# Optimization experiments

Measured on AMD Instinct MI355X. Metric: run time of the kernel, lower is better.

## Reference

```python
import jax, jax.numpy as jnp
import numpy as np

B, S, V, H, NL, NH, FF, L = 32, 256, 30522, 768, 12, 12, 3072, 9
DH = H // NH
SCALE = 1.0 / float(np.sqrt(DH))

def _ln(x, g, b, eps=1e-12):
    mu = x.mean(-1, keepdims=True)
    var = ((x - mu) ** 2).mean(-1, keepdims=True)
    return (x - mu) * jax.lax.rsqrt(var + eps) * g + b

def _crf_nll(em, tags, mask, start, end, trans):
    # em: [B,S,L] log-softmaxed emissions; tags: [B,S] int; mask: [B,S] bool
    b, s, l = em.shape
    bi = jnp.arange(b)
    em_t = jnp.swapaxes(em, 0, 1)          # [S,B,L]
    tg_t = tags.T                           # [S,B]
    m_t = mask.T.astype(em.dtype)           # [S,B]
    # numerator: score of the gold path
    score0 = start[tags[:, 0]] + em[bi, 0, tags[:, 0]]
    def num_step(sc, xs):
        e, tg, tgp, m = xs
        return sc + m * (trans[tgp, tg] + e[bi, tg]), None
    num, _ = jax.lax.scan(num_step, score0, (em_t[1:], tg_t[1:], tg_t[:-1], m_t[1:]))
    seq_ends = mask.sum(1).astype(jnp.int32) - 1
    num = num + end[tags[bi, seq_ends]]
    # denominator: log partition via forward algorithm
    alpha0 = start[None, :] + em[:, 0]      # [B,L]
    def den_step(al, xs):
        e, m = xs
        new = jax.nn.logsumexp(al[:, :, None] + trans[None] + e[:, None, :], axis=1)
        return jnp.where(m[:, None] > 0, new, al), None
    alpha, _ = jax.lax.scan(den_step, alpha0, (em_t[1:], m_t[1:]))
    den = jax.nn.logsumexp(alpha + end[None, :], axis=1)
    return -(num - den).sum()   # torchcrf reduction='sum', negated in module

def _bert_crf_loss(token_ids, token_type_ids, attention_mask, y, p):
    b, s = token_ids.shape
    h = p['word_emb'][token_ids] + p['pos_emb'][:s][None] + p['type_emb'][token_type_ids]
    h = _ln(h, p['emb_ln_g'], p['emb_ln_b'])
    bias = (1.0 - attention_mask.astype(jnp.float32))[:, None, None, :] * -1e9
    def layer(hc, lp):
        Wq, bq, Wk, bk, Wv, bv, Wo, bo, g1, bln1, W1, b1, W2, b2, g2, bln2 = lp
        q = (hc @ Wq + bq).reshape(b, s, NH, DH)
        k = (hc @ Wk + bk).reshape(b, s, NH, DH)
        v = (hc @ Wv + bv).reshape(b, s, NH, DH)
        att = jnp.einsum('bqhd,bkhd->bhqk', q, k) * SCALE + bias
        att = jax.nn.softmax(att, axis=-1)
        ctx = jnp.einsum('bhqk,bkhd->bqhd', att, v).reshape(b, s, H)
        hc = _ln(hc + ctx @ Wo + bo, g1, bln1)
        ff = jax.nn.gelu(hc @ W1 + b1) @ W2 + b2
        hc = _ln(hc + ff, g2, bln2)
        return hc, None
    stacked = (p['Wq'], p['bq'], p['Wk'], p['bk'], p['Wv'], p['bv'], p['Wo'], p['bo'],
               p['ln1_g'], p['ln1_b'], p['W1'], p['b1'], p['W2'], p['b2'], p['ln2_g'], p['ln2_b'])
    h, _ = jax.lax.scan(layer, h, stacked)
    # dropout is identity in eval; fc has no bias; LogSoftmax over labels
    logits = jax.nn.log_softmax(h @ p['fc_w'], axis=-1)   # [B,S,L]
    return _crf_nll(logits, y, attention_mask.astype(bool), p['crf_start'], p['crf_end'], p['crf_trans'])

def setup_inputs() -> dict:
    key = jax.random.key(0)
    ks = iter(jax.random.split(key, 32))
    def nrm(shape, scale=0.02):
        return (jax.random.normal(next(ks), shape, jnp.float32) * scale)
    inp = dict(
        token_ids=jax.random.randint(next(ks), (B, S), 0, V),
        token_type_ids=jnp.zeros((B, S), jnp.int32),
        attention_mask=jnp.ones((B, S), jnp.int32),
        y=jax.random.randint(next(ks), (B, S), 0, L),
        word_emb=nrm((V, H)), pos_emb=nrm((S, H)), type_emb=nrm((2, H)),
        emb_ln_g=jnp.ones(H, jnp.float32), emb_ln_b=jnp.zeros(H, jnp.float32),
        Wq=nrm((NL, H, H)), bq=jnp.zeros((NL, H), jnp.float32),
        Wk=nrm((NL, H, H)), bk=jnp.zeros((NL, H), jnp.float32),
        Wv=nrm((NL, H, H)), bv=jnp.zeros((NL, H), jnp.float32),
        Wo=nrm((NL, H, H)), bo=jnp.zeros((NL, H), jnp.float32),
        ln1_g=jnp.ones((NL, H), jnp.float32), ln1_b=jnp.zeros((NL, H), jnp.float32),
        W1=nrm((NL, H, FF)), b1=jnp.zeros((NL, FF), jnp.float32),
        W2=nrm((NL, FF, H)), b2=jnp.zeros((NL, H), jnp.float32),
        ln2_g=jnp.ones((NL, H), jnp.float32), ln2_b=jnp.zeros((NL, H), jnp.float32),
        fc_w=nrm((H, L)),
        crf_start=nrm((L,), 0.1), crf_end=nrm((L,), 0.1), crf_trans=nrm((L, L), 0.1),
    )
    return inp

def reference(token_ids, token_type_ids, attention_mask, y, word_emb, pos_emb, type_emb,
              emb_ln_g, emb_ln_b, Wq, bq, Wk, bk, Wv, bv, Wo, bo, ln1_g, ln1_b,
              W1, b1, W2, b2, ln2_g, ln2_b, fc_w, crf_start, crf_end, crf_trans):
    p = dict(word_emb=word_emb, pos_emb=pos_emb, type_emb=type_emb,
             emb_ln_g=emb_ln_g, emb_ln_b=emb_ln_b, Wq=Wq, bq=bq, Wk=Wk, bk=bk,
             Wv=Wv, bv=bv, Wo=Wo, bo=bo, ln1_g=ln1_g, ln1_b=ln1_b,
             W1=W1, b1=b1, W2=W2, b2=b2, ln2_g=ln2_g, ln2_b=ln2_b,
             fc_w=fc_w, crf_start=crf_start, crf_end=crf_end, crf_trans=crf_trans)
    return _bert_crf_loss(token_ids, token_type_ids, attention_mask, y, p)
```

## Files before the change

### kernel.cpp

```cpp
#include <hip/hip_runtime.h>
#include <math.h>

typedef unsigned short ushortT;
typedef unsigned char u8;
typedef __attribute__((ext_vector_type(4))) float f32x4;
typedef __attribute__((ext_vector_type(4))) unsigned int u32x4;
typedef __attribute__((ext_vector_type(4))) unsigned short u16x4;
typedef __attribute__((ext_vector_type(4))) int i32x4;
typedef __attribute__((ext_vector_type(8))) __bf16 bf16x8;

namespace {
constexpr int S = 256;
constexpr int H = 768;
constexpr int NLAY = 12;
constexpr int NHD = 12;
constexpr int FF = 3072;
constexpr int LBL = 9;
constexpr int DH = 64;
constexpr int BATCH = 32;
constexpr int TOKENS = BATCH * S;
constexpr int QKVN = 3 * H;
constexpr float C2 = 0.18033688011112042f;

constexpr size_t HB_OFF  = 0;
constexpr size_t QB_OFF  = HB_OFF + (size_t)TOKENS*H/2;
constexpr size_t KB_OFF  = QB_OFF + (size_t)TOKENS*H/2;
constexpr size_t VT_OFF  = KB_OFF + (size_t)TOKENS*H/2;
constexpr size_t BIG_OFF = VT_OFF + (size_t)TOKENS*H/2;
constexpr size_t WTQ_OFF = BIG_OFF + (size_t)TOKENS*FF/2;
constexpr size_t WTO_OFF = WTQ_OFF + 3*(size_t)H*H/4;
constexpr size_t WT1_OFF = WTO_OFF + (size_t)H*H/4;
constexpr size_t WT2_OFF = WT1_OFF + (size_t)H*FF/4;
constexpr size_t EM_OFF  = WT2_OFF + (size_t)H*FF/4;
constexpr size_t PART_OFF= EM_OFF + (size_t)TOKENS*LBL;
constexpr size_t BQKV_OFF= PART_OFF + 64;
constexpr size_t H8_OFF  = BQKV_OFF + (size_t)NLAY*QKVN;
constexpr size_t CT8_OFF = H8_OFF + (size_t)TOKENS*H/4;
constexpr size_t WS_FLOATS = CT8_OFF + (size_t)TOKENS*H/4;
}

__device__ __forceinline__ ushortT f2bf(float x) {
    unsigned u = __builtin_bit_cast(unsigned, x);
    u += 0x7fffu + ((u >> 16) & 1u);
    return (ushortT)(u >> 16);
}
__device__ __forceinline__ float bf2f(ushortT h) {
    unsigned u = ((unsigned)h) << 16;
    return __builtin_bit_cast(float, u);
}
__device__ __forceinline__ u8 f2fp8(float x) {
    return (u8)(__builtin_amdgcn_cvt_pk_fp8_f32(x, x, 0, false) & 0xff);
}
__device__ __forceinline__ unsigned f2fp8x4(float a, float b, float c, float d) {
    int p = __builtin_amdgcn_cvt_pk_fp8_f32(a, b, 0, false);
    p = __builtin_amdgcn_cvt_pk_fp8_f32(c, d, p, true);
    return (unsigned)p;
}

__device__ __forceinline__ float exp2i(float x) {
    float r; asm("v_exp_f32 %0, %1" : "=v"(r) : "v"(x)); return r;
}
__device__ __forceinline__ float log2i(float x) {
    float r; asm("v_log_f32 %0, %1" : "=v"(r) : "v"(x)); return r;
}

__device__ __forceinline__ float gelu_tanh(float x) {
    float u = 0.7978845608028654f * (x + 0.044715f * x * x * x);
    float t = exp2i(-2.8853900817779268f * u);
    return x / (1.0f + t);
}

__device__ __forceinline__ f32x4 mfma16(u32x4 a, u32x4 b, f32x4 c) {
    return __builtin_amdgcn_mfma_f32_16x16x32_bf16(
        __builtin_bit_cast(bf16x8, a), __builtin_bit_cast(bf16x8, b), c, 0, 0, 0);
}

__device__ __forceinline__ void gload_lds16(const ushortT* g, ushortT* l) {
    __builtin_amdgcn_global_load_lds(
        (const __attribute__((address_space(1))) unsigned int*)g,
        (__attribute__((address_space(3))) unsigned int*)l,
        16, 0, 0);
}
__device__ __forceinline__ void gload_lds16b(const u8* g, u8* l) {
    __builtin_amdgcn_global_load_lds(
        (const __attribute__((address_space(1))) unsigned int*)g,
        (__attribute__((address_space(3))) unsigned int*)l,
        16, 0, 0);
}

template<int MODE>
__global__ __launch_bounds__(256) void gemm_fp8(
    const u8* __restrict__ A, int lda,
    const u8* __restrict__ Bt, int ldb,
    const float* __restrict__ bias,
    void* __restrict__ Cv, int ldc, int K)
{
    __shared__ __align__(16) u8 As[3][128 * 64];
    __shared__ __align__(16) u8 Bs[3][128 * 64];
    const int tid = threadIdx.x;
    const int wave = tid >> 6, lane = tid & 63;

    int bxi = blockIdx.x, byi = blockIdx.y;
    {
        const int nwg = gridDim.x * gridDim.y;
        const int lin = byi * gridDim.x + bxi;
        const int cpx = nwg >> 3;
        const int sw = (lin & 7) * cpx + (lin >> 3);
        byi = sw / gridDim.x; bxi = sw - byi * gridDim.x;
    }
    const int bm = byi * 128, bn = bxi * 128;
    const u8* Ab = A + (size_t)bm * lda;
    const u8* Bb = Bt + (size_t)bn * ldb;
    const int wm = wave >> 1, wn = wave & 1;

    const int lrow = lane >> 2;
    const int lswb = ((lane & 3) ^ ((lrow >> 1) & 3)) * 16;
    const int rl = lane & 15;
    const int kg = lane >> 4;
    const int kg4 = kg << 2;
    const int key = (rl >> 1) & 3;
    const int kgh = kg >> 1, kgl8 = (kg & 1) * 8;

    f32x4 acc[4][4];
#pragma unroll
    for (int i = 0; i < 4; ++i)
#pragma unroll
        for (int j = 0; j < 4; ++j) acc[i][j] = (f32x4){0.f, 0.f, 0.f, 0.f};

    auto stage = [&](int buf, int kt) {
#pragma unroll
        for (int j = 0; j < 2; ++j) {
            int chunk = j * 4 + wave;
            gload_lds16b(Ab + (size_t)(chunk * 16 + lrow) * lda + kt * 64 + lswb,
                         &As[buf][chunk * 1024]);
        }
#pragma unroll
        for (int j = 0; j < 2; ++j) {
            int chunk = j * 4 + wave;
            gload_lds16b(Bb + (size_t)(chunk * 16 + lrow) * ldb + kt * 64 + lswb,
                         &Bs[buf][chunk * 1024]);
        }
    };

    const int nt = K >> 6;
    stage(0, 0);
    stage(1, (nt > 1) ? 1 : 0);
    int cur = 0;
    for (int t = 0; t < nt; ++t) {
        asm volatile("s_waitcnt vmcnt(4)" ::: "memory");
        __builtin_amdgcn_s_barrier();
        __builtin_amdgcn_sched_barrier(0);
#pragma unroll
        for (int ks = 0; ks < 2; ++ks) {
            long a[4], b[4];
#pragma unroll
            for (int mf = 0; mf < 4; ++mf)
                a[mf] = *(const long*)&As[cur][(wm * 64 + mf * 16 + rl) * 64 +
                                               (((ks * 2 + kgh) ^ key) << 4) + kgl8];
#pragma unroll
            for (int nf = 0; nf < 4; ++nf)
                b[nf] = *(const long*)&Bs[cur][(wn * 64 + nf * 16 + rl) * 64 +
                                               (((ks * 2 + kgh) ^ key) << 4) + kgl8];
            if (ks == 0) {
                const int nx = (t + 2 < nt) ? t + 2 : nt - 1;
                int nb = cur + 2; if (nb >= 3) nb -= 3;
                stage(nb, nx);
            }
#pragma unroll
            for (int mf = 0; mf < 4; ++mf)
#pragma unroll
                for (int nf = 0; nf < 4; ++nf)
                    acc[mf][nf] = __builtin_amdgcn_mfma_f32_16x16x32_fp8_fp8(
                        a[mf], b[nf], acc[mf][nf], 0, 0, 0);
        }
        cur = (cur + 1 == 3) ? 0 : cur + 1;
    }
    asm volatile("s_waitcnt vmcnt(0)" ::: "memory");

#pragma unroll
    for (int nf = 0; nf < 4; ++nf) {
        const int gn = bn + wn * 64 + nf * 16 + rl;
        const float bv = bias[gn];
#pragma unroll
        for (int mf = 0; mf < 4; ++mf) {
            const int gm = bm + wm * 64 + mf * 16 + kg4;
            if constexpr (MODE == 7) {
                u8* C8 = (u8*)Cv;
#pragma unroll
                for (int r = 0; r < 4; ++r)
                    C8[(size_t)(gm + r) * ldc + gn] = f2fp8(gelu_tanh(acc[mf][nf][r] + bv));
            } else if constexpr (MODE == 9) {
                const int region = gn / H;
                const int col = gn - region * H;
                if (region < 2) {
                    ushortT* o = (ushortT*)Cv + (size_t)region * TOKENS * H;
#pragma unroll
                    for (int r = 0; r < 4; ++r)
                        o[(size_t)(gm + r) * H + col] = f2bf(acc[mf][nf][r] + bv);
                } else {
                    u16x4 o;
#pragma unroll
                    for (int r = 0; r < 4; ++r) o[r] = f2bf(acc[mf][nf][r] + bv);
                    const int b_ = gm >> 8, s0 = gm & 255;
                    const int h_ = col >> 6, dh = col & 63;
                    *(u16x4*)((ushortT*)Cv + 2 * (size_t)TOKENS * H +
                              (((size_t)(b_ * NHD + h_) * DH + dh) << 8) + s0) = o;
                }
            } else {
                ushortT* Ch = (ushortT*)Cv;
#pragma unroll
                for (int r = 0; r < 4; ++r)
                    Ch[(size_t)(gm + r) * ldc + gn] = f2bf(acc[mf][nf][r] + bv);
            }
        }
    }
}

template<int WM, int WN, int MODE>
__global__ __launch_bounds__(256) void gemm_mfma(
    const ushortT* __restrict__ A, int lda, long long sAo, long long sAi,
    const ushortT* __restrict__ Bt, int ldb, long long sBo, long long sBi,
    const float* __restrict__ bias,
    void* __restrict__ Cv, int ldc, long long sCo, long long sCi,
    int K, int innerN)
{
    constexpr int BM = WM * 64, BN = WN * 64;
    __shared__ __align__(16) ushortT As[3][BM * 32];
    __shared__ __align__(16) ushortT Bs[3][BN * 32];
    const int tid = threadIdx.x;
    const int wave = tid >> 6, lane = tid & 63;
    const int ob = blockIdx.z / innerN, ib = blockIdx.z - ob * innerN;

    const int bm = blockIdx.y * BM, bn = blockIdx.x * BN;
    const ushortT* Ab = A + ob * sAo + ib * sAi + (size_t)bm * lda;
    const ushortT* Bb = Bt + ob * sBo + ib * sBi + (size_t)bn * ldb;
    const int wm = wave / WN, wn = wave - wm * WN;

    const int lrow = lane >> 2;
    const int lsw16 = ((lane & 3) ^ ((lrow >> 1) & 3)) * 8;
    const int rl = lane & 15;
    const int kg4 = (lane >> 4) << 2;
    const int ksw = ((lane >> 4) ^ ((rl >> 1) & 3)) << 3;

    f32x4 acc[4][4];
#pragma unroll
    for (int i = 0; i < 4; ++i)
#pragma unroll
        for (int j = 0; j < 4; ++j) acc[i][j] = (f32x4){0.f, 0.f, 0.f, 0.f};

    auto stage = [&](int buf, int k0) {
#pragma unroll
        for (int j = 0; j < WM; ++j) {
            int chunk = j * 4 + wave;
            gload_lds16(Ab + (size_t)(chunk * 16 + lrow) * lda + k0 + lsw16,
                        &As[buf][chunk * 512]);
        }
#pragma unroll
        for (int j = 0; j < WN; ++j) {
            int chunk = j * 4 + wave;
            gload_lds16(Bb + (size_t)(chunk * 16 + lrow) * ldb + k0 + lsw16,
                        &Bs[buf][chunk * 512]);
        }
    };

    const int nt = K >> 5;
    stage(0, 0);
    stage(1, ((nt > 1) ? 1 : 0) << 5);
    int cur = 0;
    for (int t = 0; t < nt; ++t) {
        if constexpr (WM + WN == 4)
            asm volatile("s_waitcnt vmcnt(4)" ::: "memory");
        else
            asm volatile("s_waitcnt vmcnt(5)" ::: "memory");
        __builtin_amdgcn_s_barrier();
        __builtin_amdgcn_sched_barrier(0);
        u32x4 a[4], b[4];
#pragma unroll
        for (int mf = 0; mf < 4; ++mf)
            a[mf] = *(const u32x4*)&As[cur][(wm * 64 + mf * 16 + rl) * 32 + ksw];
#pragma unroll
        for (int nf = 0; nf < 4; ++nf)
            b[nf] = *(const u32x4*)&Bs[cur][(wn * 64 + nf * 16 + rl) * 32 + ksw];
        {
            const int nx = (t + 2 < nt) ? t + 2 : nt - 1;
            int nb = cur + 2; if (nb >= 3) nb -= 3;
            stage(nb, nx << 5);
        }
#pragma unroll
        for (int mf = 0; mf < 4; ++mf)
#pragma unroll
            for (int nf = 0; nf < 4; ++nf)
                acc[mf][nf] = mfma16(a[mf], b[nf], acc[mf][nf]);
        cur = (cur + 1 == 3) ? 0 : cur + 1;
    }
    asm volatile("s_waitcnt vmcnt(0)" ::: "memory");

    if constexpr (MODE == 6) {
        ushortT* Ch = (ushortT*)Cv + ob * sCo + ib * sCi;
        __shared__ float red6[2][4][64];
        const int* mrow = (const int*)bias + ob * S;
        float mb[4];
#pragma unroll
        for (int nf = 0; nf < 4; ++nf)
            mb[nf] = mrow[bn + wn * 64 + nf * 16 + rl] ? 0.f : -8e9f;
        float pm[4][4];
#pragma unroll
        for (int mf = 0; mf < 4; ++mf)
#pragma unroll
            for (int r = 0; r < 4; ++r) pm[mf][r] = -1e30f;
#pragma unroll
        for (int mf = 0; mf < 4; ++mf)
#pragma unroll
            for (int nf = 0; nf < 4; ++nf)
#pragma unroll
                for (int r = 0; r < 4; ++r) {
                    acc[mf][nf][r] += mb[nf];
                    pm[mf][r] = fmaxf(pm[mf][r], acc[mf][nf][r]);
                }
#pragma unroll
        for (int mf = 0; mf < 4; ++mf)
#pragma unroll
            for (int r = 0; r < 4; ++r) {
                float v = pm[mf][r];
                v = fmaxf(v, __shfl_xor(v, 1));
                v = fmaxf(v, __shfl_xor(v, 2));
                v = fmaxf(v, __shfl_xor(v, 4));
                v = fmaxf(v, __shfl_xor(v, 8));
                pm[mf][r] = v;
            }
        if (rl == 0) {
#pragma unroll
            for (int mf = 0; mf < 4; ++mf)
#pragma unroll
                for (int r = 0; r < 4; ++r)
                    red6[0][wn][mf * 16 + kg4 + r] = pm[mf][r];
        }
        __syncthreads();
        float Mx[4][4];
#pragma unroll
        for (int mf = 0; mf < 4; ++mf)
#pragma unroll
            for (int r = 0; r < 4; ++r) {
                const int row = mf * 16 + kg4 + r;
                Mx[mf][r] = fmaxf(fmaxf(red6[0][0][row], red6[0][1][row]),
                                  fmaxf(red6[0][2][row], red6[0][3][row]));
            }
        float ps[4][4];
#pragma unroll
        for (int mf = 0; mf < 4; ++mf)
#pragma unroll
            for (int r = 0; r < 4; ++r) ps[mf][r] = 0.f;
#pragma unroll
        for (int mf = 0; mf < 4; ++mf)
#pragma unroll
            for (int nf = 0; nf < 4; ++nf)
#pragma unroll
                for (int r = 0; r < 4; ++r) {
                    float e = exp2i(C2 * (acc[mf][nf][r] - Mx[mf][r]));
                    acc[mf][nf][r] = e;
                    ps[mf][r] += e;
                }
#pragma unroll
        for (int mf = 0; mf < 4; ++mf)
#pragma unroll
            for (int r = 0; r < 4; ++r) {
                float v = ps[mf][r];
                v += __shfl_xor(v, 1);
                v += __shfl_xor(v, 2);
                v += __shfl_xor(v, 4);
                v += __shfl_xor(v, 8);
                ps[mf][r] = v;
            }
        if (rl == 0) {
#pragma unroll
            for (int mf = 0; mf < 4; ++mf)
#pragma unroll
                for (int r = 0; r < 4; ++r)
                    red6[1][wn][mf * 16 + kg4 + r] = ps[mf][r];
        }
        __syncthreads();
#pragma unroll
        for (int mf = 0; mf < 4; ++mf) {
            float inv[4];
#pragma unroll
            for (int r = 0; r < 4; ++r) {
                const int row = mf * 16 + kg4 + r;
                inv[r] = 1.0f / (red6[1][0][row] + red6[1][1][row] +
                                 red6[1][2][row] + red6[1][3][row]);
            }
#pragma unroll
            for (int nf = 0; nf < 4; ++nf) {
                const int gn = bn + wn * 64 + nf * 16 + rl;
                const int gm = bm + mf * 16 + kg4;
#pragma unroll
                for (int r = 0; r < 4; ++r)
                    Ch[(size_t)(gm + r) * ldc + gn] = f2bf(acc[mf][nf][r] * inv[r]);
            }
        }
    } else {
        u8* C8 = (u8*)Cv + ob * sCo + ib * sCi;
#pragma unroll
        for (int nf = 0; nf < 4; ++nf) {
            int gn = bn + wn * 64 + nf * 16 + rl;
#pragma unroll
            for (int mf = 0; mf < 4; ++mf) {
                int gm = bm + wm * 64 + mf * 16 + kg4;
#pragma unroll
                for (int r = 0; r < 4; ++r)
                    C8[(size_t)(gm + r) * ldc + gn] = f2fp8(acc[mf][nf][r]);
            }
        }
    }
}

__global__ __launch_bounds__(256) void transpose_all_k(
    const float* __restrict__ Wq, const float* __restrict__ Wk,
    const float* __restrict__ Wv, const float* __restrict__ Wo,
    const float* __restrict__ W1, const float* __restrict__ W2,
    u8* __restrict__ wtqkv8, u8* __restrict__ wto8,
    u8* __restrict__ wt1, u8* __restrict__ wt2)
{
    int idx = blockIdx.x;
    const float* W; int R, C, tr, tc; u8* WT8;
    if (idx < 2304) {
        int mat = idx / 576, t = idx - mat * 576;
        tr = t / 24; tc = t - tr * 24; R = 768; C = 768;
        W = mat == 0 ? Wq : mat == 1 ? Wk : mat == 2 ? Wv : Wo;
        WT8 = mat < 3 ? wtqkv8 + (size_t)mat * 768 * 768 : wto8;
    } else if (idx < 4608) {
        int t = idx - 2304; tr = t / 96; tc = t - tr * 96;
        R = 768; C = 3072; W = W1; WT8 = wt1;
    } else {
        int t = idx - 4608; tr = t / 24; tc = t - tr * 24;
        R = 3072; C = 768; W = W2; WT8 = wt2;
    }
    int r0 = tr * 32, c0 = tc * 32;
    __shared__ float tl[32][33];
    int trd = threadIdx.x >> 3;
    int tc4 = (threadIdx.x & 7) * 4;
    const float4 v = *(const float4*)(W + (size_t)(r0 + trd) * C + c0 + tc4);
    tl[trd][tc4 + 0] = v.x; tl[trd][tc4 + 1] = v.y;
    tl[trd][tc4 + 2] = v.z; tl[trd][tc4 + 3] = v.w;
    __syncthreads();
    unsigned p = f2fp8x4(tl[tc4 + 0][trd], tl[tc4 + 1][trd],
                         tl[tc4 + 2][trd], tl[tc4 + 3][trd]);
    *(unsigned*)(WT8 + (size_t)(c0 + trd) * R + r0 + tc4) = p;
}

__global__ __launch_bounds__(256) void pack_bias_k(
    const float* __restrict__ bq, const float* __restrict__ bk,
    const float* __restrict__ bv, float* __restrict__ out)
{
    int l = blockIdx.x / 3, r = blockIdx.x - (blockIdx.x / 3) * 3;
    const float* src = r == 0 ? bq : r == 1 ? bk : bv;
#pragma unroll
    for (int j = 0; j < 3; ++j) {
        int d = threadIdx.x + 256 * j;
        out[(size_t)l * QKVN + r * H + d] = src[(size_t)l * H + d];
    }
}

__global__ __launch_bounds__(256) void embed_ln_k(
    const int* __restrict__ ids, const int* __restrict__ tts,
    const float* __restrict__ wemb, const float* __restrict__ pemb,
    const float* __restrict__ temb, const float* __restrict__ g,
    const float* __restrict__ bp, ushortT* __restrict__ hb, u8* __restrict__ h8)
{
    const int tok = blockIdx.x * 4 + (threadIdx.x >> 6);
    const int lane = threadIdx.x & 63;
    const int d0 = lane * 12;
    const int spos = tok & (S - 1);
    const int id = ids[tok], tt = tts[tok];
    const float* wr = wemb + (size_t)id * H + d0;
    const float* pr = pemb + (size_t)spos * H + d0;
    const float* tr = temb + (size_t)tt * H + d0;
    float x[12]; float s = 0.f, ss = 0.f;
#pragma unroll
    for (int j = 0; j < 3; ++j) {
        float4 a = *(const float4*)(wr + j * 4);
        float4 b = *(const float4*)(pr + j * 4);
        float4 c = *(const float4*)(tr + j * 4);
        float v0 = a.x + b.x + c.x, v1 = a.y + b.y + c.y;
        float v2 = a.z + b.z + c.z, v3 = a.w + b.w + c.w;
        x[j*4+0] = v0; x[j*4+1] = v1; x[j*4+2] = v2; x[j*4+3] = v3;
        s += v0 + v1 + v2 + v3;
        ss += v0*v0 + v1*v1 + v2*v2 + v3*v3;
    }
#pragma unroll
    for (int m = 32; m; m >>= 1) { s += __shfl_xor(s, m); ss += __shfl_xor(ss, m); }
    float mu = s * (1.f / H);
    float var = ss * (1.f / H) - mu * mu;
    float rs = rsqrtf(var + 1e-12f);
#pragma unroll
    for (int j = 0; j < 3; ++j) {
        float4 gv = *(const float4*)(g + d0 + j * 4);
        float4 bv = *(const float4*)(bp + d0 + j * 4);
        float y0 = (x[j*4+0] - mu) * rs * gv.x + bv.x;
        float y1 = (x[j*4+1] - mu) * rs * gv.y + bv.y;
        float y2 = (x[j*4+2] - mu) * rs * gv.z + bv.z;
        float y3 = (x[j*4+3] - mu) * rs * gv.w + bv.w;
        u16x4 o;
        o[0] = f2bf(y0); o[1] = f2bf(y1); o[2] = f2bf(y2); o[3] = f2bf(y3);
        *(u16x4*)(hb + (size_t)tok * H + d0 + j * 4) = o;
        *(unsigned*)(h8 + (size_t)tok * H + d0 + j * 4) = f2fp8x4(y0, y1, y2, y3);
    }
}

__global__ __launch_bounds__(256) void add_ln_k(
    ushortT* __restrict__ hb, const ushortT* __restrict__ add,
    const float* __restrict__ g, const float* __restrict__ bp,
    u8* __restrict__ h8)
{
    const int tok = blockIdx.x * 4 + (threadIdx.x >> 6);
    const int lane = threadIdx.x & 63;
    const int d0 = lane * 12;
    const size_t base = (size_t)tok * H + d0;
    float x[12]; float s = 0.f, ss = 0.f;
#pragma unroll
    for (int j = 0; j < 3; ++j) {
        u16x4 hv = *(const u16x4*)(hb + base + j * 4);
        u16x4 av = *(const u16x4*)(add + base + j * 4);
#pragma unroll
        for (int q = 0; q < 4; ++q) {
            float v = bf2f(hv[q]) + bf2f(av[q]);
            x[j*4+q] = v; s += v; ss += v * v;
        }
    }
#pragma unroll
    for (int m = 32; m; m >>= 1) { s += __shfl_xor(s, m); ss += __shfl_xor(ss, m); }
    float mu = s * (1.f / H);
    float var = ss * (1.f / H) - mu * mu;
    float rs = rsqrtf(var + 1e-12f);
#pragma unroll
    for (int j = 0; j < 3; ++j) {
        float4 gv = *(const float4*)(g + d0 + j * 4);
        float4 bv = *(const float4*)(bp + d0 + j * 4);
        float y0 = (x[j*4+0] - mu) * rs * gv.x + bv.x;
        float y1 = (x[j*4+1] - mu) * rs * gv.y + bv.y;
        float y2 = (x[j*4+2] - mu) * rs * gv.z + bv.z;
        float y3 = (x[j*4+3] - mu) * rs * gv.w + bv.w;
        u16x4 o;
        o[0] = f2bf(y0); o[1] = f2bf(y1); o[2] = f2bf(y2); o[3] = f2bf(y3);
        *(u16x4*)(hb + base + j * 4) = o;
        *(unsigned*)(h8 + base + j * 4) = f2fp8x4(y0, y1, y2, y3);
    }
}

__global__ __launch_bounds__(256) void logits_k(
    const ushortT* __restrict__ hb, const float* __restrict__ fcw,
    float* __restrict__ em)
{
    int tok = blockIdx.x, tid = threadIdx.x;
    float p[LBL];
#pragma unroll
    for (int l = 0; l < LBL; ++l) p[l] = 0.f;
    const ushortT* hr = hb + (size_t)tok * H;
#pragma unroll
    for (int j = 0; j < 3; ++j) {
        int d = tid + 256 * j;
        float hv = bf2f(hr[d]);
        const float* fr = fcw + (size_t)d * LBL;
#pragma unroll
        for (int l = 0; l < LBL; ++l) p[l] = fmaf(hv, fr[l], p[l]);
    }
    __shared__ float ls[4][LBL];
    __shared__ float lg[LBL];
    __shared__ float lse;
#pragma unroll
    for (int l = 0; l < LBL; ++l) {
        float v = p[l];
#pragma unroll
        for (int m = 32; m; m >>= 1) v += __shfl_xor(v, m);
        if ((tid & 63) == 0) ls[tid >> 6][l] = v;
    }
    __syncthreads();
    if (tid < LBL) lg[tid] = ls[0][tid] + ls[1][tid] + ls[2][tid] + ls[3][tid];
    __syncthreads();
    if (tid == 0) {
        float mx = lg[0];
#pragma unroll
        for (int j = 1; j < LBL; ++j) mx = fmaxf(mx, lg[j]);
        float sm = 0.f;
#pragma unroll
        for (int j = 0; j < LBL; ++j) sm += expf(lg[j] - mx);
        lse = mx + logf(sm);
    }
    __syncthreads();
    if (tid < LBL) em[(size_t)tok * LBL + tid] = lg[tid] - lse;
}

__global__ __launch_bounds__(64) void crf_k(
    const float* __restrict__ em, const int* __restrict__ tags,
    const int* __restrict__ mask, const float* __restrict__ sp,
    const float* __restrict__ ep, const float* __restrict__ trans,
    float* __restrict__ partial)
{
    constexpr float LOG2E = 1.4426950408889634f;
    constexpr float LN2   = 0.6931471805599453f;
    int b = blockIdx.x, t = threadIdx.x;
    __shared__ float eml[S * LBL];
    __shared__ int mkl[S];
    const float* emb = em + (size_t)b * S * LBL;
    const int* tg = tags + (size_t)b * S;
    const int* mk = mask + (size_t)b * S;

    for (int i = t * 4; i < S * LBL; i += 256) {
        float4 v = *(const float4*)&emb[i];
        v.x *= LOG2E; v.y *= LOG2E; v.z *= LOG2E; v.w *= LOG2E;
        *(float4*)&eml[i] = v;
    }
    *(i32x4*)&mkl[t * 4] = *(const i32x4*)&mk[t * 4];

    int cnt = 0; float ns = 0.f;
    for (int i = t; i < S; i += 64) {
        int m = mk[i];
        cnt += (m != 0);
        if (i >= 1 && m)
            ns += trans[tg[i - 1] * LBL + tg[i]] + emb[(size_t)i * LBL + tg[i]];
    }
#pragma unroll
    for (int m = 32; m; m >>= 1) { cnt += __shfl_xor(cnt, m); ns += __shfl_xor(ns, m); }
    float num = ns + sp[tg[0]] + emb[tg[0]] + ep[tg[cnt - 1]];

    int tt = t < LBL ? t : 0;
    float trc2[LBL];
#pragma unroll
    for (int i = 0; i < LBL; ++i) trc2[i] = trans[i * LBL + tt] * LOG2E;

    __syncthreads();

    float alpha2 = (t < LBL) ? sp[t] * LOG2E + eml[t] : -1e30f;
    for (int step = 1; step < S; ++step) {
        float av[LBL];
#pragma unroll
        for (int i = 0; i < LBL; ++i) av[i] = __shfl(alpha2, i) + trc2[i];
        float mx = av[0];
#pragma unroll
        for (int i = 1; i < LBL; ++i) mx = fmaxf(mx, av[i]);
        float sm = 0.f;
#pragma unroll
        for (int i = 0; i < LBL; ++i) sm += exp2i(av[i] - mx);
        float na = mx + log2i(sm) + eml[step * LBL + tt];
        alpha2 = (mkl[step] && t < LBL) ? na : alpha2;
    }
    float z = (t < LBL) ? alpha2 + ep[t] * LOG2E : -1e30f;
    float mx = z;
#pragma unroll
    for (int m = 8; m; m >>= 1) mx = fmaxf(mx, __shfl_xor(mx, m));
    float sm = exp2i(z - mx);
#pragma unroll
    for (int m = 8; m; m >>= 1) sm += __shfl_xor(sm, m);
    if (t == 0) partial[b] = (mx + log2i(sm)) * LN2 - num;
}

__global__ void finalize_k(const float* __restrict__ partial, float* __restrict__ out) {
    float s = 0.f;
    for (int i = 0; i < BATCH; ++i) s += partial[i];
    out[0] = s;
}

__global__ void sentinel_k(float* out) { out[0] = -12345.0f; }

extern "C" void kernel_launch(void* const* d_in, const int* in_sizes, int n_in,
                              void* d_out, int out_size, void* d_ws, size_t ws_size,
                              hipStream_t stream) {
    (void)in_sizes; (void)n_in; (void)out_size;
    const int* token_ids  = (const int*)d_in[0];
    const int* token_type = (const int*)d_in[1];
    const int* amask      = (const int*)d_in[2];
    const int* y          = (const int*)d_in[3];
    const float* wemb = (const float*)d_in[4];
    const float* pemb = (const float*)d_in[5];
    const float* temb = (const float*)d_in[6];
    const float* eg   = (const float*)d_in[7];
    const float* eb   = (const float*)d_in[8];
    const float* Wq = (const float*)d_in[9];
    const float* bq = (const float*)d_in[10];
    const float* Wk = (const float*)d_in[11];
    const float* bk = (const float*)d_in[12];
    const float* Wv = (const float*)d_in[13];
    const float* bv = (const float*)d_in[14];
    const float* Wo = (const float*)d_in[15];
    const float* bo = (const float*)d_in[16];
    const float* ln1g = (const float*)d_in[17];
    const float* ln1b = (const float*)d_in[18];
    const float* W1 = (const float*)d_in[19];
    const float* b1 = (const float*)d_in[20];
    const float* W2 = (const float*)d_in[21];
    const float* b2 = (const float*)d_in[22];
    const float* ln2g = (const float*)d_in[23];
    const float* ln2b = (const float*)d_in[24];
    const float* fcw = (const float*)d_in[25];
    const float* crf_s = (const float*)d_in[26];
    const float* crf_e = (const float*)d_in[27];
    const float* crf_t = (const float*)d_in[28];

    if (ws_size < WS_FLOATS * sizeof(float)) {
        sentinel_k<<<1, 1, 0, stream>>>((float*)d_out);
        return;
    }

    float* ws = (float*)d_ws;
    ushortT* hb    = (ushortT*)(ws + HB_OFF);
    ushortT* qb    = (ushortT*)(ws + QB_OFF);
    ushortT* kb    = (ushortT*)(ws + KB_OFF);
    ushortT* vt    = (ushortT*)(ws + VT_OFF);
    ushortT* big   = (ushortT*)(ws + BIG_OFF);
    u8*      big8  = (u8*)(ws + BIG_OFF);
    u8*      wtq8  = (u8*)(ws + WTQ_OFF);
    u8*      wto8  = (u8*)(ws + WTO_OFF);
    u8*      wt1   = (u8*)(ws + WT1_OFF);
    u8*      wt2   = (u8*)(ws + WT2_OFF);
    float*   embuf = ws + EM_OFF;
    float*   part  = ws + PART_OFF;
    float*   bqkv  = ws + BQKV_OFF;
    u8*      h8    = (u8*)(ws + H8_OFF);
    u8*      ctx8  = (u8*)(ws + CT8_OFF);

    pack_bias_k<<<NLAY * 3, 256, 0, stream>>>(bq, bk, bv, bqkv);
    embed_ln_k<<<TOKENS / 4, 256, 0, stream>>>(token_ids, token_type, wemb, pemb,
                                               temb, eg, eb, hb, h8);

    constexpr long long HH = (long long)H * H;
    constexpr long long HF = (long long)H * FF;
    constexpr long long TOKH = (long long)S * H;
    constexpr long long ATT_B = (long long)NHD * S * S;
    constexpr long long ATT_H = (long long)S * S;
    constexpr long long VT_B = (long long)NHD * DH * S;
    constexpr long long VT_H = (long long)DH * S;

    dim3 gQKV(QKVN / 128, TOKENS / 128, 1);
    dim3 gProj(H / 128, TOKENS / 128, 1);
    dim3 gFF1(FF / 128, TOKENS / 128, 1);
    dim3 gScores(1, S / 64, BATCH * NHD);
    dim3 gPV(1, 1, BATCH * NHD);

    for (int l = 0; l < NLAY; ++l) {
        transpose_all_k<<<6912, 256, 0, stream>>>(
            Wq + l * HH, Wk + l * HH, Wv + l * HH, Wo + l * HH,
            W1 + l * HF, W2 + l * HF, wtq8, wto8, wt1, wt2);

        gemm_fp8<9><<<gQKV, 256, 0, stream>>>(
            h8, H, wtq8, H, bqkv + (size_t)l * QKVN, qb, H, H);

        gemm_mfma<1,4,6><<<gScores, 256, 0, stream>>>(
            qb, H, TOKH, DH, kb, H, TOKH, DH, (const float*)amask,
            big, S, ATT_B, ATT_H, DH, NHD);

        gemm_mfma<4,1,10><<<gPV, 256, 0, stream>>>(
            big, S, ATT_B, ATT_H, vt, S, VT_B, VT_H, nullptr,
            ctx8, H, TOKH, DH, S, NHD);

        gemm_fp8<8><<<gProj, 256, 0, stream>>>(
            ctx8, H, wto8, H, bo + l * H, kb, H, H);

        add_ln_k<<<TOKENS / 4, 256, 0, stream>>>(hb, kb, ln1g + l * H, ln1b + l * H, h8);

        gemm_fp8<7><<<gFF1, 256, 0, stream>>>(
            h8, H, wt1, H, b1 + (long long)l * FF, big8, FF, H);

        gemm_fp8<8><<<gProj, 256, 0, stream>>>(
            big8, FF, wt2, FF, b2 + l * H, qb, H, FF);

        add_ln_k<<<TOKENS / 4, 256, 0, stream>>>(hb, qb, ln2g + l * H, ln2b + l * H, h8);
    }

    logits_k<<<TOKENS, 256, 0, stream>>>(hb, fcw, embuf);
    crf_k<<<BATCH, 64, 0, stream>>>(embuf, y, amask, crf_s, crf_e, crf_t, part);
    finalize_k<<<1, 1, 0, stream>>>(part, (float*)d_out);
}
```

Before: 2.585 ms.

## Move attention QK and PV GEMMs from bf16 to fp8 with a unified batched kernel

Merges the bf16 batched GEMM and the fp8 dense GEMM into one templated fp8 kernel that supports strided batching and variable warp tiling. The QKV projection now writes Q, K and transposed V as fp8, and the attention score/softmax stage writes its probabilities as fp8, so the QK^T and PV products use fp8 MFMA with half the memory traffic of bf16. The workspace layout shrinks to match. This trades more precision loss in attention against lower bandwidth and higher MFMA throughput.

```diff
diff --git a/kernel.cpp b/kernel.cpp
--- a/kernel.cpp
+++ b/kernel.cpp
@@ -7,7 +7,6 @@
 typedef __attribute__((ext_vector_type(4))) unsigned int u32x4;
 typedef __attribute__((ext_vector_type(4))) unsigned short u16x4;
 typedef __attribute__((ext_vector_type(4))) int i32x4;
-typedef __attribute__((ext_vector_type(8))) __bf16 bf16x8;
 
 namespace {
 constexpr int S = 256;
@@ -23,11 +22,10 @@
 constexpr float C2 = 0.18033688011112042f;
 
 constexpr size_t HB_OFF  = 0;
-constexpr size_t QB_OFF  = HB_OFF + (size_t)TOKENS*H/2;
-constexpr size_t KB_OFF  = QB_OFF + (size_t)TOKENS*H/2;
-constexpr size_t VT_OFF  = KB_OFF + (size_t)TOKENS*H/2;
-constexpr size_t BIG_OFF = VT_OFF + (size_t)TOKENS*H/2;
-constexpr size_t WTQ_OFF = BIG_OFF + (size_t)TOKENS*FF/2;
+constexpr size_t OB_OFF  = HB_OFF + (size_t)TOKENS*H/2;
+constexpr size_t Q8_OFF  = OB_OFF + (size_t)TOKENS*H/2;
+constexpr size_t BIG_OFF = Q8_OFF + 3*(size_t)TOKENS*H/4;
+constexpr size_t WTQ_OFF = BIG_OFF + (size_t)TOKENS*FF/4;
 constexpr size_t WTO_OFF = WTQ_OFF + 3*(size_t)H*H/4;
 constexpr size_t WT1_OFF = WTO_OFF + (size_t)H*H/4;
 constexpr size_t WT2_OFF = WT1_OFF + (size_t)H*FF/4;
@@ -70,17 +68,6 @@
     return x / (1.0f + t);
 }
 
-__device__ __forceinline__ f32x4 mfma16(u32x4 a, u32x4 b, f32x4 c) {
-    return __builtin_amdgcn_mfma_f32_16x16x32_bf16(
-        __builtin_bit_cast(bf16x8, a), __builtin_bit_cast(bf16x8, b), c, 0, 0, 0);
-}
-
-__device__ __forceinline__ void gload_lds16(const ushortT* g, ushortT* l) {
-    __builtin_amdgcn_global_load_lds(
-        (const __attribute__((address_space(1))) unsigned int*)g,
-        (__attribute__((address_space(3))) unsigned int*)l,
-        16, 0, 0);
-}
 __device__ __forceinline__ void gload_lds16b(const u8* g, u8* l) {
     __builtin_amdgcn_global_load_lds(
         (const __attribute__((address_space(1))) unsigned int*)g,
@@ -88,30 +75,33 @@
         16, 0, 0);
 }
 
-template<int MODE>
-__global__ __launch_bounds__(256) void gemm_fp8(
-    const u8* __restrict__ A, int lda,
-    const u8* __restrict__ Bt, int ldb,
+template<int WM, int WN, int MODE>
+__global__ __launch_bounds__(256) void gemm_fp8b(
+    const u8* __restrict__ A, int lda, long long sAo, long long sAi,
+    const u8* __restrict__ Bt, int ldb, long long sBo, long long sBi,
     const float* __restrict__ bias,
-    void* __restrict__ Cv, int ldc, int K)
+    void* __restrict__ Cv, int ldc, long long sCo, long long sCi,
+    int K, int innerN)
 {
-    __shared__ __align__(16) u8 As[3][128 * 64];
-    __shared__ __align__(16) u8 Bs[3][128 * 64];
+    constexpr int BM = WM * 64, BN = WN * 64;
+    __shared__ __align__(16) u8 As[3][BM * 64];
+    __shared__ __align__(16) u8 Bs[3][BN * 64];
     const int tid = threadIdx.x;
     const int wave = tid >> 6, lane = tid & 63;
+    const int ob = blockIdx.z / innerN, ib = blockIdx.z - ob * innerN;
 
     int bxi = blockIdx.x, byi = blockIdx.y;
-    {
+    if (gridDim.z == 1) {
         const int nwg = gridDim.x * gridDim.y;
         const int lin = byi * gridDim.x + bxi;
         const int cpx = nwg >> 3;
         const int sw = (lin & 7) * cpx + (lin >> 3);
         byi = sw / gridDim.x; bxi = sw - byi * gridDim.x;
     }
-    const int bm = byi * 128, bn = bxi * 128;
-    const u8* Ab = A + (size_t)bm * lda;
-    const u8* Bb = Bt + (size_t)bn * ldb;
-    const int wm = wave >> 1, wn = wave & 1;
+    const int bm = byi * BM, bn = bxi * BN;
+    const u8* Ab = A + ob * sAo + ib * sAi + (size_t)bm * lda;
+    const u8* Bb = Bt + ob * sBo + ib * sBi + (size_t)bn * ldb;
+    const int wm = wave / WN, wn = wave - wm * WN;
 
     const int lrow = lane >> 2;
     const int lswb = ((lane & 3) ^ ((lrow >> 1) & 3)) * 16;
@@ -129,13 +119,13 @@
 
     auto stage = [&](int buf, int kt) {
 #pragma unroll
-        for (int j = 0; j < 2; ++j) {
+        for (int j = 0; j < WM; ++j) {
             int chunk = j * 4 + wave;
             gload_lds16b(Ab + (size_t)(chunk * 16 + lrow) * lda + kt * 64 + lswb,
                          &As[buf][chunk * 1024]);
         }
 #pragma unroll
-        for (int j = 0; j < 2; ++j) {
+        for (int j = 0; j < WN; ++j) {
             int chunk = j * 4 + wave;
             gload_lds16b(Bb + (size_t)(chunk * 16 + lrow) * ldb + kt * 64 + lswb,
                          &Bs[buf][chunk * 1024]);
@@ -147,7 +137,10 @@
     stage(1, (nt > 1) ? 1 : 0);
     int cur = 0;
     for (int t = 0; t < nt; ++t) {
-        asm volatile("s_waitcnt vmcnt(4)" ::: "memory");
+        if constexpr (WM + WN == 4)
+            asm volatile("s_waitcnt vmcnt(4)" ::: "memory");
+        else
+            asm volatile("s_waitcnt vmcnt(5)" ::: "memory");
         __builtin_amdgcn_s_barrier();
         __builtin_amdgcn_sched_barrier(0);
 #pragma unroll
@@ -177,126 +170,8 @@
     }
     asm volatile("s_waitcnt vmcnt(0)" ::: "memory");
 
-#pragma unroll
-    for (int nf = 0; nf < 4; ++nf) {
-        const int gn = bn + wn * 64 + nf * 16 + rl;
-        const float bv = bias[gn];
-#pragma unroll
-        for (int mf = 0; mf < 4; ++mf) {
-            const int gm = bm + wm * 64 + mf * 16 + kg4;
-            if constexpr (MODE == 7) {
-                u8* C8 = (u8*)Cv;
-#pragma unroll
-                for (int r = 0; r < 4; ++r)
-                    C8[(size_t)(gm + r) * ldc + gn] = f2fp8(gelu_tanh(acc[mf][nf][r] + bv));
-            } else if constexpr (MODE == 9) {
-                const int region = gn / H;
-                const int col = gn - region * H;
-                if (region < 2) {
-                    ushortT* o = (ushortT*)Cv + (size_t)region * TOKENS * H;
-#pragma unroll
-                    for (int r = 0; r < 4; ++r)
-                        o[(size_t)(gm + r) * H + col] = f2bf(acc[mf][nf][r] + bv);
-                } else {
-                    u16x4 o;
-#pragma unroll
-                    for (int r = 0; r < 4; ++r) o[r] = f2bf(acc[mf][nf][r] + bv);
-                    const int b_ = gm >> 8, s0 = gm & 255;
-                    const int h_ = col >> 6, dh = col & 63;
-                    *(u16x4*)((ushortT*)Cv + 2 * (size_t)TOKENS * H +
-                              (((size_t)(b_ * NHD + h_) * DH + dh) << 8) + s0) = o;
-                }
-            } else {
-                ushortT* Ch = (ushortT*)Cv;
-#pragma unroll
-                for (int r = 0; r < 4; ++r)
-                    Ch[(size_t)(gm + r) * ldc + gn] = f2bf(acc[mf][nf][r] + bv);
-            }
-        }
-    }
-}
-
-template<int WM, int WN, int MODE>
-__global__ __launch_bounds__(256) void gemm_mfma(
-    const ushortT* __restrict__ A, int lda, long long sAo, long long sAi,
-    const ushortT* __restrict__ Bt, int ldb, long long sBo, long long sBi,
-    const float* __restrict__ bias,
-    void* __restrict__ Cv, int ldc, long long sCo, long long sCi,
-    int K, int innerN)
-{
-    constexpr int BM = WM * 64, BN = WN * 64;
-    __shared__ __align__(16) ushortT As[3][BM * 32];
-    __shared__ __align__(16) ushortT Bs[3][BN * 32];
-    const int tid = threadIdx.x;
-    const int wave = tid >> 6, lane = tid & 63;
-    const int ob = blockIdx.z / innerN, ib = blockIdx.z - ob * innerN;
-
-    const int bm = blockIdx.y * BM, bn = blockIdx.x * BN;
-    const ushortT* Ab = A + ob * sAo + ib * sAi + (size_t)bm * lda;
-    const ushortT* Bb = Bt + ob * sBo + ib * sBi + (size_t)bn * ldb;
-    const int wm = wave / WN, wn = wave - wm * WN;
-
-    const int lrow = lane >> 2;
-    const int lsw16 = ((lane & 3) ^ ((lrow >> 1) & 3)) * 8;
-    const int rl = lane & 15;
-    const int kg4 = (lane >> 4) << 2;
-    const int ksw = ((lane >> 4) ^ ((rl >> 1) & 3)) << 3;
-
-    f32x4 acc[4][4];
-#pragma unroll
-    for (int i = 0; i < 4; ++i)
-#pragma unroll
-        for (int j = 0; j < 4; ++j) acc[i][j] = (f32x4){0.f, 0.f, 0.f, 0.f};
-
-    auto stage = [&](int buf, int k0) {
-#pragma unroll
-        for (int j = 0; j < WM; ++j) {
-            int chunk = j * 4 + wave;
-            gload_lds16(Ab + (size_t)(chunk * 16 + lrow) * lda + k0 + lsw16,
-                        &As[buf][chunk * 512]);
-        }
-#pragma unroll
-        for (int j = 0; j < WN; ++j) {
-            int chunk = j * 4 + wave;
-            gload_lds16(Bb + (size_t)(chunk * 16 + lrow) * ldb + k0 + lsw16,
-                        &Bs[buf][chunk * 512]);
-        }
-    };
-
-    const int nt = K >> 5;
-    stage(0, 0);
-    stage(1, ((nt > 1) ? 1 : 0) << 5);
-    int cur = 0;
-    for (int t = 0; t < nt; ++t) {
-        if constexpr (WM + WN == 4)
-            asm volatile("s_waitcnt vmcnt(4)" ::: "memory");
-        else
-            asm volatile("s_waitcnt vmcnt(5)" ::: "memory");
-        __builtin_amdgcn_s_barrier();
-        __builtin_amdgcn_sched_barrier(0);
-        u32x4 a[4], b[4];
-#pragma unroll
-        for (int mf = 0; mf < 4; ++mf)
-            a[mf] = *(const u32x4*)&As[cur][(wm * 64 + mf * 16 + rl) * 32 + ksw];
-#pragma unroll
-        for (int nf = 0; nf < 4; ++nf)
-            b[nf] = *(const u32x4*)&Bs[cur][(wn * 64 + nf * 16 + rl) * 32 + ksw];
-        {
-            const int nx = (t + 2 < nt) ? t + 2 : nt - 1;
-            int nb = cur + 2; if (nb >= 3) nb -= 3;
-            stage(nb, nx << 5);
-        }
-#pragma unroll
-        for (int mf = 0; mf < 4; ++mf)
-#pragma unroll
-            for (int nf = 0; nf < 4; ++nf)
-                acc[mf][nf] = mfma16(a[mf], b[nf], acc[mf][nf]);
-        cur = (cur + 1 == 3) ? 0 : cur + 1;
-    }
-    asm volatile("s_waitcnt vmcnt(0)" ::: "memory");
-
     if constexpr (MODE == 6) {
-        ushortT* Ch = (ushortT*)Cv + ob * sCo + ib * sCi;
+        u8* C8 = (u8*)Cv + ob * sCo + ib * sCi;
         __shared__ float red6[2][4][64];
         const int* mrow = (const int*)bias + ob * S;
         float mb[4];
@@ -394,20 +269,51 @@
                 const int gm = bm + mf * 16 + kg4;
 #pragma unroll
                 for (int r = 0; r < 4; ++r)
-                    Ch[(size_t)(gm + r) * ldc + gn] = f2bf(acc[mf][nf][r] * inv[r]);
+                    C8[(size_t)(gm + r) * ldc + gn] = f2fp8(acc[mf][nf][r] * inv[r]);
             }
         }
     } else {
-        u8* C8 = (u8*)Cv + ob * sCo + ib * sCi;
 #pragma unroll
         for (int nf = 0; nf < 4; ++nf) {
-            int gn = bn + wn * 64 + nf * 16 + rl;
+            const int gn = bn + wn * 64 + nf * 16 + rl;
+            float bv = 0.f;
+            if constexpr (MODE != 10) bv = bias[gn];
 #pragma unroll
             for (int mf = 0; mf < 4; ++mf) {
-                int gm = bm + wm * 64 + mf * 16 + kg4;
-#pragma unroll
-                for (int r = 0; r < 4; ++r)
-                    C8[(size_t)(gm + r) * ldc + gn] = f2fp8(acc[mf][nf][r]);
+                const int gm = bm + wm * 64 + mf * 16 + kg4;
+                if constexpr (MODE == 7) {
+                    u8* C8 = (u8*)Cv;
+#pragma unroll
+                    for (int r = 0; r < 4; ++r)
+                        C8[(size_t)(gm + r) * ldc + gn] =
+                            f2fp8(gelu_tanh(acc[mf][nf][r] + bv));
+                } else if constexpr (MODE == 8) {
+                    ushortT* Ch = (ushortT*)Cv;
+#pragma unroll
+                    for (int r = 0; r < 4; ++r)
+                        Ch[(size_t)(gm + r) * ldc + gn] = f2bf(acc[mf][nf][r] + bv);
+                } else if constexpr (MODE == 9) {
+                    const int region = gn / H;
+                    const int col = gn - region * H;
+                    if (region < 2) {
+                        u8* o = (u8*)Cv + (size_t)region * TOKENS * H;
+#pragma unroll
+                        for (int r = 0; r < 4; ++r)
+                            o[(size_t)(gm + r) * H + col] = f2fp8(acc[mf][nf][r] + bv);
+                    } else {
+                        const int b_ = gm >> 8, s0 = gm & 255;
+                        const int h_ = col >> 6, dh = col & 63;
+                        *(unsigned*)((u8*)Cv + 2 * (size_t)TOKENS * H +
+                                     (((size_t)(b_ * NHD + h_) * DH + dh) << 8) + s0) =
+                            f2fp8x4(acc[mf][nf][0] + bv, acc[mf][nf][1] + bv,
+                                    acc[mf][nf][2] + bv, acc[mf][nf][3] + bv);
+                    }
+                } else {
+                    u8* C8 = (u8*)Cv + ob * sCo + ib * sCi;
+#pragma unroll
+                    for (int r = 0; r < 4; ++r)
+                        C8[(size_t)(gm + r) * ldc + gn] = f2fp8(acc[mf][nf][r]);
+                }
             }
         }
     }
@@ -702,10 +608,10 @@
 
     float* ws = (float*)d_ws;
     ushortT* hb    = (ushortT*)(ws + HB_OFF);
-    ushortT* qb    = (ushortT*)(ws + QB_OFF);
-    ushortT* kb    = (ushortT*)(ws + KB_OFF);
-    ushortT* vt    = (ushortT*)(ws + VT_OFF);
-    ushortT* big   = (ushortT*)(ws + BIG_OFF);
+    ushortT* obuf  = (ushortT*)(ws + OB_OFF);
+    u8*      q8    = (u8*)(ws + Q8_OFF);
+    u8*      k8    = q8 + (size_t)TOKENS * H;
+    u8*      vt8   = q8 + 2 * (size_t)TOKENS * H;
     u8*      big8  = (u8*)(ws + BIG_OFF);
     u8*      wtq8  = (u8*)(ws + WTQ_OFF);
     u8*      wto8  = (u8*)(ws + WTO_OFF);
@@ -723,7 +629,7 @@
 
     constexpr long long HH = (long long)H * H;
     constexpr long long HF = (long long)H * FF;
-    constexpr long long TOKH = (long long)S * H;
+    constexpr long long SH = (long long)S * H;
     constexpr long long ATT_B = (long long)NHD * S * S;
     constexpr long long ATT_H = (long long)S * S;
     constexpr long long VT_B = (long long)NHD * DH * S;
@@ -740,29 +646,30 @@
             Wq + l * HH, Wk + l * HH, Wv + l * HH, Wo + l * HH,
             W1 + l * HF, W2 + l * HF, wtq8, wto8, wt1, wt2);
 
-        gemm_fp8<9><<<gQKV, 256, 0, stream>>>(
-            h8, H, wtq8, H, bqkv + (size_t)l * QKVN, qb, H, H);
-
-        gemm_mfma<1,4,6><<<gScores, 256, 0, stream>>>(
-            qb, H, TOKH, DH, kb, H, TOKH, DH, (const float*)amask,
-            big, S, ATT_B, ATT_H, DH, NHD);
-
-        gemm_mfma<4,1,10><<<gPV, 256, 0, stream>>>(
-            big, S, ATT_B, ATT_H, vt, S, VT_B, VT_H, nullptr,
-            ctx8, H, TOKH, DH, S, NHD);
-
-        gemm_fp8<8><<<gProj, 256, 0, stream>>>(
-            ctx8, H, wto8, H, bo + l * H, kb, H, H);
-
-        add_ln_k<<<TOKENS / 4, 256, 0, stream>>>(hb, kb, ln1g + l * H, ln1b + l * H, h8);
-
-        gemm_fp8<7><<<gFF1, 256, 0, stream>>>(
-            h8, H, wt1, H, b1 + (long long)l * FF, big8, FF, H);
-
-        gemm_fp8<8><<<gProj, 256, 0, stream>>>(
-            big8, FF, wt2, FF, b2 + l * H, qb, H, FF);
-
-        add_ln_k<<<TOKENS / 4, 256, 0, stream>>>(hb, qb, ln2g + l * H, ln2b + l * H, h8);
+        gemm_fp8b<2,2,9><<<gQKV, 256, 0, stream>>>(
+            h8, H, 0, 0, wtq8, H, 0, 0, bqkv + (size_t)l * QKVN,
+            q8, H, 0, 0, H, 1);
+
+        gemm_fp8b<1,4,6><<<gScores, 256, 0, stream>>>(
+            q8, H, SH, DH, k8, H, SH, DH, (const float*)amask,
+            big8, S, ATT_B, ATT_H, DH, NHD);
+
+        gemm_fp8b<4,1,10><<<gPV, 256, 0, stream>>>(
+            big8, S, ATT_B, ATT_H, vt8, S, VT_B, VT_H, nullptr,
+            ctx8, H, SH, DH, S, NHD);
+
+        gemm_fp8b<2,2,8><<<gProj, 256, 0, stream>>>(
+            ctx8, H, 0, 0, wto8, H, 0, 0, bo + l * H, obuf, H, 0, 0, H, 1);
+
+        add_ln_k<<<TOKENS / 4, 256, 0, stream>>>(hb, obuf, ln1g + l * H, ln1b + l * H, h8);
+
+        gemm_fp8b<2,2,7><<<gFF1, 256, 0, stream>>>(
+            h8, H, 0, 0, wt1, H, 0, 0, b1 + (long long)l * FF, big8, FF, 0, 0, H, 1);
+
+        gemm_fp8b<2,2,8><<<gProj, 256, 0, stream>>>(
+            big8, FF, 0, 0, wt2, FF, 0, 0, b2 + l * H, obuf, H, 0, 0, FF, 1);
+
+        add_ln_k<<<TOKENS / 4, 256, 0, stream>>>(hb, obuf, ln2g + l * H, ln2b + l * H, h8);
     }
 
     logits_k<<<TOKENS, 256, 0, stream>>>(hb, fcw, embuf);
```

New measurement: 2.535 ms. Within noise of the previous version (-1.9%).
